# Kernel optimization log

Hardware: AMD Instinct MI355X
Metric: run time of the kernel (lower is better)

Reference implementation:

```python
import jax, jax.numpy as jnp
import numpy as np
from jax import lax

# Dense per-batch layout [B, N, 3]; PyG MLP realized as Linear(+ReLU on all but last layer);
# BatchNorm omitted (eval-mode BN with identity stats is an absorbable affine).
DIMS = {"sa1": [3, 64, 64, 128], "sa2": [131, 128, 128, 256], "sa3": [259, 256, 256, 512], "sa4": [515, 512, 1024]}
B, N, K = 8, 4096, 64  # batch clouds, points per cloud, max neighbors (from radius(..., max_num_neighbors=64))


def setup_inputs() -> dict:
    key = jax.random.key(0)
    inp = {"pos": jax.random.normal(jax.random.fold_in(key, 0), (B, N, 3), jnp.float32)}
    c = 1
    for name, ch in DIMS.items():
        for i in range(len(ch) - 1):
            inp[f"{name}_w{i}"] = jax.random.normal(jax.random.fold_in(key, c), (ch[i], ch[i + 1]), jnp.float32) / np.sqrt(ch[i])
            inp[f"{name}_b{i}"] = jnp.zeros((ch[i + 1],), jnp.float32)
            c += 1
    return inp


def _mlp(x, params):
    n = len(params)
    for i, (W, b) in enumerate(params):
        x = x @ W + b
        if i < n - 1:  # plain last layer (PyG MLP plain_last=True)
            x = jax.nn.relu(x)
    return x


def _fps(pos, n_sample):
    # farthest point sampling, deterministic start at index 0; pos [N,3]
    Np = pos.shape[0]
    def step(carry, _):
        min_d, cur = carry
        d = jnp.sum((pos - pos[cur]) ** 2, axis=-1)
        min_d = jnp.minimum(min_d, d)
        return (min_d, jnp.argmax(min_d).astype(jnp.int32)), cur
    _, idx = lax.scan(step, (jnp.full((Np,), 1e30, pos.dtype), jnp.int32(0)), None, length=n_sample)
    return idx  # [n_sample]


def _sa(x, pos, ratio, r, params):
    # SAModule: fps -> radius ball query (K nearest within r) -> PointNetConv (gather-MLP-scatter-max)
    S = int(pos.shape[1] * ratio)
    idx = jax.vmap(lambda p: _fps(p, S))(pos)                       # [B,S]
    pos_dst = jnp.take_along_axis(pos, idx[:, :, None], axis=1)     # [B,S,3]
    d2 = jnp.sum((pos_dst[:, :, None, :] - pos[:, None, :, :]) ** 2, axis=-1)  # [B,S,N]
    negd, nidx = lax.top_k(-d2, K)                                  # K nearest neighbors
    valid = (-negd) < r * r                                         # within ball radius (>=1: self at d=0)
    pos_j = jax.vmap(lambda p, i: p[i])(pos, nidx)                  # [B,S,K,3]
    rel = pos_j - pos_dst[:, :, None, :]
    if x is None:
        feat = rel
    else:
        x_j = jax.vmap(lambda a, i: a[i])(x, nidx)                  # [B,S,K,F]
        feat = jnp.concatenate([x_j, rel], axis=-1)
    h = _mlp(feat, params)                                          # [B,S,K,C]
    h = jnp.where(valid[..., None], h, -1e30)
    return jnp.max(h, axis=2), pos_dst                              # scatter-max over neighbors


def _backbone(pos, P):
    x1, pos1 = _sa(None, pos, 0.25, 0.2, P["sa1"])
    x2, pos2 = _sa(x1, pos1, 0.25, 0.4, P["sa2"])
    x3, pos3 = _sa(x2, pos2, 0.25, 0.8, P["sa3"])
    h = _mlp(jnp.concatenate([x3, pos3], axis=-1), P["sa4"])        # GlobalSAModule
    return jnp.max(h, axis=1)                                       # global_max_pool -> [B,1024]


def reference(pos, sa1_w0, sa1_b0, sa1_w1, sa1_b1, sa1_w2, sa1_b2, sa2_w0, sa2_b0, sa2_w1, sa2_b1, sa2_w2, sa2_b2, sa3_w0, sa3_b0, sa3_w1, sa3_b1, sa3_w2, sa3_b2, sa4_w0, sa4_b0, sa4_w1, sa4_b1):
    P = {
        "sa1": [(sa1_w0, sa1_b0), (sa1_w1, sa1_b1), (sa1_w2, sa1_b2)],
        "sa2": [(sa2_w0, sa2_b0), (sa2_w1, sa2_b1), (sa2_w2, sa2_b2)],
        "sa3": [(sa3_w0, sa3_b0), (sa3_w1, sa3_b1), (sa3_w2, sa3_b2)],
        "sa4": [(sa4_w0, sa4_b0), (sa4_w1, sa4_b1)],
    }
    return _backbone(pos, P)
```

## Files before the change

### kernel.cpp

```cpp
#include <hip/hip_runtime.h>

#define DEV __device__ __forceinline__

DEV float d2_exact(float ax, float ay, float az, float bx, float by, float bz) {
    float dx = __fadd_rn(ax, -bx);
    float dy = __fadd_rn(ay, -by);
    float dz = __fadd_rn(az, -bz);
    return __fadd_rn(__fadd_rn(__fmul_rn(dx, dx), __fmul_rn(dy, dy)), __fmul_rn(dz, dz));
}

DEV unsigned long long umax64(unsigned long long a, unsigned long long b) { return a > b ? a : b; }
DEV unsigned long long umin64(unsigned long long a, unsigned long long b) { return a < b ? a : b; }

template <int CTRL>
DEV float dpp_fmax(float x) {
    const int xi = __float_as_int(x);
    const int yi = __builtin_amdgcn_update_dpp(xi, xi, CTRL, 0xF, 0xF, false);
    return fmaxf(x, __int_as_float(yi));
}

DEV float wave_fmax_bcast(float x) {
    x = dpp_fmax<0x111>(x);
    x = dpp_fmax<0x112>(x);
    x = dpp_fmax<0x114>(x);
    x = dpp_fmax<0x118>(x);
    x = dpp_fmax<0x142>(x);
    x = dpp_fmax<0x143>(x);
    return __int_as_float(__builtin_amdgcn_readlane(__float_as_int(x), 63));
}

template <int N, int S, int T>
__global__ __launch_bounds__(T) void fps_kernel(const float* __restrict__ pos,
                                                float* __restrict__ pos_out) {
    constexpr int C  = N / T;
    constexpr int NW = T / 64;
    __shared__ float sx[N], sy[N], sz[N];
    __shared__ unsigned long long sred[2][NW];
    const int b = blockIdx.x, t = threadIdx.x;
    const float* p = pos + (size_t)b * N * 3;
    for (int i = t; i < N; i += T) { sx[i] = p[3*i]; sy[i] = p[3*i+1]; sz[i] = p[3*i+2]; }
    __syncthreads();
    float px[C], py[C], pz[C], md[C];
    const int base = t * C;
#pragma unroll
    for (int i = 0; i < C; i++) { px[i]=sx[base+i]; py[i]=sy[base+i]; pz[i]=sz[base+i]; md[i]=1e30f; }
    float cx = sx[0], cy = sy[0], cz = sz[0];
    const int lane = t & 63, wave = t >> 6;
    for (int s = 0; s < S; s++) {
        if (t == 0) {
            float* po = pos_out + ((size_t)b * S + s) * 3;
            po[0] = cx; po[1] = cy; po[2] = cz;
        }
        float bv = -1.0f; int bi = 0;
#pragma unroll
        for (int i = 0; i < C; i++) {
            float d = d2_exact(px[i], py[i], pz[i], cx, cy, cz);
            float m = fminf(md[i], d);
            md[i] = m;
            if (m > bv) { bv = m; bi = base + i; }
        }
        const float wm = wave_fmax_bcast(bv);
        const unsigned long long eq = __ballot(bv == wm);
        const int srcl = __ffsll(eq) - 1;
        const int wbi  = __builtin_amdgcn_readlane(bi, srcl);
        if (lane == 0)
            sred[s & 1][wave] = ((unsigned long long)__float_as_uint(wm) << 32) |
                                (unsigned long long)(unsigned int)(~wbi);
        __syncthreads();
        unsigned long long v = sred[s & 1][0];
#pragma unroll
        for (int w = 1; w < NW; w++) v = umax64(v, sred[s & 1][w]);
        const int cur = (int)(~(unsigned int)v);
        cx = sx[cur]; cy = sy[cur]; cz = sz[cur];
    }
}

template <int NSRC, int T>
__global__ __launch_bounds__(T) void ballq_kernel(const float* __restrict__ pos_src,
                                                  const float* __restrict__ pos_dst,
                                                  const int S, const float rsq,
                                                  int* __restrict__ nidx, int* __restrict__ ncnt) {
    __shared__ float d2s[NSRC];
    __shared__ int scnt, sfill;
    __shared__ unsigned long long sred[T / 64];
    const int bs = blockIdx.x, t = threadIdx.x;
    const int b = bs / S;
    const float* pd = pos_dst + (size_t)bs * 3;
    const float qx = pd[0], qy = pd[1], qz = pd[2];
    const float* ps = pos_src + (size_t)b * NSRC * 3;
    if (t == 0) { scnt = 0; sfill = 0; }
    __syncthreads();
    int lc = 0;
    for (int j = t; j < NSRC; j += T) {
        float d2 = d2_exact(ps[3*j], ps[3*j+1], ps[3*j+2], qx, qy, qz);
        d2s[j] = d2;
        lc += (d2 < rsq) ? 1 : 0;
    }
    if (lc) atomicAdd(&scnt, lc);
    __syncthreads();
    const int c = scnt;
    int* mi = nidx + (size_t)bs * 64;
    if (c <= 64) {
        if (t == 0) ncnt[bs] = c;
        for (int j = t; j < NSRC; j += T) {
            if (d2s[j] < rsq) { int p = atomicAdd(&sfill, 1); mi[p] = j; }
        }
    } else {
        if (t == 0) ncnt[bs] = 64;
        const int lane = t & 63, wave = t >> 6;
        for (int k = 0; k < 64; k++) {
            unsigned long long best = ~0ULL;
            for (int j = t; j < NSRC; j += T) {
                unsigned long long key =
                    ((unsigned long long)__float_as_uint(d2s[j]) << 32) | (unsigned int)j;
                best = umin64(best, key);
            }
#pragma unroll
            for (int o = 32; o >= 1; o >>= 1) best = umin64(best, __shfl_xor(best, o, 64));
            if (lane == 0) sred[wave] = best;
            __syncthreads();
            if (t == 0) {
                unsigned long long v = sred[0];
                for (int w = 1; w < T / 64; w++) v = umin64(v, sred[w]);
                int j = (int)(unsigned int)v;
                mi[k] = j;
                d2s[j] = __uint_as_float(0x7F800000u);
            }
            __syncthreads();
        }
    }
}

#define LP 68

template <int RPT>
DEV void fma_step(const float* __restrict__ inT, const float (*wt)[64],
                  const int cig, const int ci, const int tr, const int tc,
                  float (&acc)[RPT][4]) {
    const float4 w = *(const float4*)(&wt[ci][4 * tc]);
    const float wv[4] = {w.x, w.y, w.z, w.w};
    if constexpr (RPT == 4) {
        const float4 a = *(const float4*)(inT + (size_t)cig * LP + 4 * tr);
        const float av[4] = {a.x, a.y, a.z, a.w};
#pragma unroll
        for (int i = 0; i < 4; i++)
#pragma unroll
            for (int j = 0; j < 4; j++) acc[i][j] = fmaf(av[i], wv[j], acc[i][j]);
    } else {
        const float2 a = *(const float2*)(inT + (size_t)cig * LP + 2 * tr);
        const float av[2] = {a.x, a.y};
#pragma unroll
        for (int i = 0; i < 2; i++)
#pragma unroll
            for (int j = 0; j < 4; j++) acc[i][j] = fmaf(av[i], wv[j], acc[i][j]);
    }
}

template <int CIN, int COUT, bool RELU, int TT>
DEV void gemm_tile(const float* __restrict__ inT, const float* __restrict__ W,
                   const float* __restrict__ bias, float* __restrict__ outT,
                   float (*wt)[64], const int t) {
    constexpr int RPT  = 1024 / TT;
    constexpr int NCH  = CIN / 32;
    constexpr int TAIL = CIN % 32;
    const int tc = t & 15, tr = t >> 4;
    for (int co0 = 0; co0 < COUT; co0 += 64) {
        float acc[RPT][4] = {};
        for (int ch = 0; ch < NCH; ch++) {
            const int ci0 = ch * 32;
            __syncthreads();
            for (int e = t; e < 2048; e += TT) {
                const int co = e & 63, ci = e >> 6;
                wt[ci][co] = W[(size_t)(ci0 + ci) * COUT + co0 + co];
            }
            __syncthreads();
#pragma unroll 4
            for (int ci = 0; ci < 32; ci++)
                fma_step<RPT>(inT, (const float(*)[64])wt, ci0 + ci, ci, tr, tc, acc);
        }
        if constexpr (TAIL > 0) {
            constexpr int ci0 = NCH * 32;
            __syncthreads();
            for (int e = t; e < TAIL * 64; e += TT) {
                const int co = e & 63, ci = e >> 6;
                wt[ci][co] = W[(size_t)(ci0 + ci) * COUT + co0 + co];
            }
            __syncthreads();
#pragma unroll
            for (int ci = 0; ci < TAIL; ci++)
                fma_step<RPT>(inT, (const float(*)[64])wt, ci0 + ci, ci, tr, tc, acc);
        }
#pragma unroll
        for (int j = 0; j < 4; j++) {
            const float bj = bias[co0 + 4 * tc + j];
            if constexpr (RPT == 4) {
                float4 o;
                o.x = acc[0][j] + bj; o.y = acc[1][j] + bj;
                o.z = acc[2][j] + bj; o.w = acc[3][j] + bj;
                if (RELU) {
                    o.x = fmaxf(o.x, 0.f); o.y = fmaxf(o.y, 0.f);
                    o.z = fmaxf(o.z, 0.f); o.w = fmaxf(o.w, 0.f);
                }
                *(float4*)(outT + (size_t)(co0 + 4 * tc + j) * LP + 4 * tr) = o;
            } else {
                float2 o;
                o.x = acc[0][j] + bj; o.y = acc[1][j] + bj;
                if (RELU) { o.x = fmaxf(o.x, 0.f); o.y = fmaxf(o.y, 0.f); }
                *(float2*)(outT + (size_t)(co0 + 4 * tc + j) * LP + 2 * tr) = o;
            }
        }
    }
}

template <int CIN, int COUT, int TT>
DEV void gemm_maxout(const float* __restrict__ inT, const float* __restrict__ W,
                     const float* __restrict__ bias, float* __restrict__ outg,
                     float (*wt)[64], float (*colred)[64], const int t, const int c) {
    constexpr int RPT = 1024 / TT;
    constexpr int NW  = TT / 64;
    constexpr int NCH = CIN / 32;
    const int tc = t & 15, tr = t >> 4, wave = t >> 6;
    for (int co0 = 0; co0 < COUT; co0 += 64) {
        float acc[RPT][4] = {};
        for (int ch = 0; ch < NCH; ch++) {
            const int ci0 = ch * 32;
            __syncthreads();
            for (int e = t; e < 2048; e += TT) {
                const int co = e & 63, ci = e >> 6;
                wt[ci][co] = W[(size_t)(ci0 + ci) * COUT + co0 + co];
            }
            __syncthreads();
#pragma unroll 4
            for (int ci = 0; ci < 32; ci++)
                fma_step<RPT>(inT, (const float(*)[64])wt, ci0 + ci, ci, tr, tc, acc);
        }
        float vr[4];
#pragma unroll
        for (int j = 0; j < 4; j++) {
            const float bj = bias[co0 + 4 * tc + j];
            float m = -1e30f;
#pragma unroll
            for (int i = 0; i < RPT; i++) {
                const float v = acc[i][j] + bj;
                if (RPT * tr + i < c) m = fmaxf(m, v);
            }
            m = fmaxf(m, __shfl_xor(m, 16, 64));
            m = fmaxf(m, __shfl_xor(m, 32, 64));
            vr[j] = m;
        }
        if ((t & 48) == 0) {
#pragma unroll
            for (int j = 0; j < 4; j++) colred[wave][4 * tc + j] = vr[j];
        }
        __syncthreads();
        if (t < 64) {
            float m = colred[0][t];
#pragma unroll
            for (int w = 1; w < NW; w++) m = fmaxf(m, colred[w][t]);
            outg[co0 + t] = m;
        }
        __syncthreads();
    }
}

template <int CX, int C0, int C1, int C2, int NSRC, int TT>
__global__ __launch_bounds__(TT) void sa_conv_kernel(
    const float* __restrict__ x_src, const float* __restrict__ pos_src,
    const float* __restrict__ pos_dst, const int* __restrict__ nidx,
    const int* __restrict__ ncnt,
    const float* __restrict__ w0, const float* __restrict__ b0,
    const float* __restrict__ w1, const float* __restrict__ b1,
    const float* __restrict__ w2, const float* __restrict__ b2,
    float* __restrict__ x_out, const int S) {
    constexpr int CIN = CX + 3;
    constexpr int AR  = (CIN > C1) ? CIN : C1;
    __shared__ float bufA[AR * LP];
    __shared__ float bufB[C0 * LP];
    __shared__ float wt[32][64];
    __shared__ float colred[TT / 64][64];
    const int bs = blockIdx.x, t = threadIdx.x;
    const int b = bs / S;
    const int c = ncnt[bs];
    const int* ni = nidx + (size_t)bs * 64;
    const float* pd = pos_dst + (size_t)bs * 3;
    const float qx = pd[0], qy = pd[1], qz = pd[2];
    if constexpr (CX > 0) {
        constexpr int LG = (CX == 256) ? 8 : 7;
#pragma unroll 4
        for (int e = t; e < 64 * CX; e += TT) {
            const int ci = e & (CX - 1), k = e >> LG;
            float v = 0.f;
            if (k < c) v = x_src[((size_t)b * NSRC + ni[k]) * CX + ci];
            bufA[(size_t)ci * LP + k] = v;
        }
    }
    for (int e = t; e < 192; e += TT) {
        const int k = e & 63, ci = e >> 6;
        float v = 0.f;
        if (k < c) {
            const float* pj = pos_src + ((size_t)b * NSRC + ni[k]) * 3;
            v = (ci == 0 ? pj[0] - qx : (ci == 1 ? pj[1] - qy : pj[2] - qz));
        }
        bufA[(size_t)(CX + ci) * LP + k] = v;
    }
    __syncthreads();
    gemm_tile<CIN, C0, true, TT>(bufA, w0, b0, bufB, wt, t);
    __syncthreads();
    gemm_tile<C0, C1, true, TT>(bufB, w1, b1, bufA, wt, t);
    __syncthreads();
    gemm_maxout<C1, C2, TT>(bufA, w2, b2, x_out + (size_t)bs * C2, wt, colred, t, c);
}

__global__ __launch_bounds__(256) void gsa1_kernel(const float* __restrict__ x3,
                                                   const float* __restrict__ pos3,
                                                   const float* __restrict__ w0,
                                                   const float* __restrict__ b0,
                                                   float* __restrict__ h1) {
    __shared__ float at[32][LP];
    __shared__ float wt[32][64];
    const int b = blockIdx.x >> 3, co0 = (blockIdx.x & 7) * 64;
    const int t = threadIdx.x, tc = t & 15, tr = t >> 4;
    float acc[4][4] = {};
    for (int ci0 = 0; ci0 < 515; ci0 += 32) {
        const int cc = (515 - ci0) < 32 ? (515 - ci0) : 32;
        __syncthreads();
        for (int e = t; e < cc * 64; e += 256) {
            const int k = e & 63, ci = e >> 6, cig = ci0 + ci;
            at[ci][k] = (cig < 512) ? x3[((size_t)b * 64 + k) * 512 + cig]
                                    : pos3[((size_t)b * 64 + k) * 3 + (cig - 512)];
        }
        for (int e = t; e < cc * 64; e += 256) {
            const int co = e & 63, ci = e >> 6;
            wt[ci][co] = w0[(size_t)(ci0 + ci) * 512 + co0 + co];
        }
        __syncthreads();
#pragma unroll 4
        for (int ci = 0; ci < 32; ci++) {
            if (ci >= cc) break;
            const float4 a = *(const float4*)&at[ci][4 * tr];
            const float4 w = *(const float4*)&wt[ci][4 * tc];
            const float av[4] = {a.x, a.y, a.z, a.w};
            const float wv[4] = {w.x, w.y, w.z, w.w};
#pragma unroll
            for (int i = 0; i < 4; i++)
#pragma unroll
                for (int j = 0; j < 4; j++) acc[i][j] = fmaf(av[i], wv[j], acc[i][j]);
        }
    }
#pragma unroll
    for (int j = 0; j < 4; j++) {
        const float bj = b0[co0 + 4 * tc + j];
#pragma unroll
        for (int i = 0; i < 4; i++) {
            float v = acc[i][j] + bj;
            v = fmaxf(v, 0.f);
            h1[((size_t)b * 64 + 4 * tr + i) * 512 + co0 + 4 * tc + j] = v;
        }
    }
}

__global__ __launch_bounds__(256) void gsa2_kernel(const float* __restrict__ h1,
                                                   const float* __restrict__ w1,
                                                   const float* __restrict__ b1,
                                                   float* __restrict__ out) {
    __shared__ float at[32][LP];
    __shared__ float wt[32][64];
    __shared__ float colred[4][64];
    const int b = blockIdx.x >> 4, co0 = (blockIdx.x & 15) * 64;
    const int t = threadIdx.x, tc = t & 15, tr = t >> 4, wave = t >> 6;
    float acc[4][4] = {};
    for (int ci0 = 0; ci0 < 512; ci0 += 32) {
        __syncthreads();
        for (int e = t; e < 32 * 64; e += 256) {
            const int k = e & 63, ci = e >> 6;
            at[ci][k] = h1[((size_t)b * 64 + k) * 512 + ci0 + ci];
        }
        for (int e = t; e < 32 * 64; e += 256) {
            const int co = e & 63, ci = e >> 6;
            wt[ci][co] = w1[(size_t)(ci0 + ci) * 1024 + co0 + co];
        }
        __syncthreads();
#pragma unroll 4
        for (int ci = 0; ci < 32; ci++) {
            const float4 a = *(const float4*)&at[ci][4 * tr];
            const float4 w = *(const float4*)&wt[ci][4 * tc];
            const float av[4] = {a.x, a.y, a.z, a.w};
            const float wv[4] = {w.x, w.y, w.z, w.w};
#pragma unroll
            for (int i = 0; i < 4; i++)
#pragma unroll
                for (int j = 0; j < 4; j++) acc[i][j] = fmaf(av[i], wv[j], acc[i][j]);
        }
    }
    float vr[4];
#pragma unroll
    for (int j = 0; j < 4; j++) {
        const float bj = b1[co0 + 4 * tc + j];
        float m = -1e30f;
#pragma unroll
        for (int i = 0; i < 4; i++) m = fmaxf(m, acc[i][j] + bj);
        m = fmaxf(m, __shfl_xor(m, 16, 64));
        m = fmaxf(m, __shfl_xor(m, 32, 64));
        vr[j] = m;
    }
    if ((t & 48) == 0) {
#pragma unroll
        for (int j = 0; j < 4; j++) colred[wave][4 * tc + j] = vr[j];
    }
    __syncthreads();
    if (t < 64) {
        const float m = fmaxf(fmaxf(colred[0][t], colred[1][t]),
                              fmaxf(colred[2][t], colred[3][t]));
        out[(size_t)b * 1024 + co0 + t] = m;
    }
}

extern "C" void kernel_launch(void* const* d_in, const int* in_sizes, int n_in,
                              void* d_out, int out_size, void* d_ws, size_t ws_size,
                              hipStream_t stream) {
    (void)in_sizes; (void)n_in; (void)out_size; (void)ws_size;
    const float* pos    = (const float*)d_in[0];
    const float* sa1_w0 = (const float*)d_in[1];  const float* sa1_b0 = (const float*)d_in[2];
    const float* sa1_w1 = (const float*)d_in[3];  const float* sa1_b1 = (const float*)d_in[4];
    const float* sa1_w2 = (const float*)d_in[5];  const float* sa1_b2 = (const float*)d_in[6];
    const float* sa2_w0 = (const float*)d_in[7];  const float* sa2_b0 = (const float*)d_in[8];
    const float* sa2_w1 = (const float*)d_in[9];  const float* sa2_b1 = (const float*)d_in[10];
    const float* sa2_w2 = (const float*)d_in[11]; const float* sa2_b2 = (const float*)d_in[12];
    const float* sa3_w0 = (const float*)d_in[13]; const float* sa3_b0 = (const float*)d_in[14];
    const float* sa3_w1 = (const float*)d_in[15]; const float* sa3_b1 = (const float*)d_in[16];
    const float* sa3_w2 = (const float*)d_in[17]; const float* sa3_b2 = (const float*)d_in[18];
    const float* sa4_w0 = (const float*)d_in[19]; const float* sa4_b0 = (const float*)d_in[20];
    const float* sa4_w1 = (const float*)d_in[21]; const float* sa4_b1 = (const float*)d_in[22];
    float* out = (float*)d_out;
    char* ws = (char*)d_ws;

    float* pos1 = (float*)(ws + 0);
    float* pos2 = (float*)(ws + 98304);
    float* pos3 = (float*)(ws + 122880);
    float* x1   = (float*)(ws + 129024);
    float* x2   = (float*)(ws + 4323328);
    float* x3   = (float*)(ws + 6420480);
    int* nidx1  = (int*)(ws + 7469056);
    int* ncnt1  = (int*)(ws + 9566208);
    int* nidx2  = (int*)(ws + 9598976);
    int* ncnt2  = (int*)(ws + 10123264);
    int* nidx3  = (int*)(ws + 10131456);
    int* ncnt3  = (int*)(ws + 10262528);
    float* h1g  = (float*)(ws + 10264576);

    const float rsq1 = (float)(0.2 * 0.2);
    const float rsq2 = (float)(0.4 * 0.4);
    const float rsq3 = (float)(0.8 * 0.8);

    fps_kernel<4096, 1024, 256><<<dim3(8), dim3(256), 0, stream>>>(pos, pos1);
    fps_kernel<1024, 256, 256><<<dim3(8), dim3(256), 0, stream>>>(pos1, pos2);
    fps_kernel<256, 64, 256><<<dim3(8), dim3(256), 0, stream>>>(pos2, pos3);

    ballq_kernel<4096, 256><<<dim3(8 * 1024), dim3(256), 0, stream>>>(pos, pos1, 1024, rsq1, nidx1, ncnt1);
    ballq_kernel<1024, 256><<<dim3(8 * 256), dim3(256), 0, stream>>>(pos1, pos2, 256, rsq2, nidx2, ncnt2);
    ballq_kernel<256, 256><<<dim3(8 * 64), dim3(256), 0, stream>>>(pos2, pos3, 64, rsq3, nidx3, ncnt3);

    sa_conv_kernel<0, 64, 64, 128, 4096, 256><<<dim3(8 * 1024), dim3(256), 0, stream>>>(
        nullptr, pos, pos1, nidx1, ncnt1, sa1_w0, sa1_b0, sa1_w1, sa1_b1, sa1_w2, sa1_b2, x1, 1024);
    sa_conv_kernel<128, 128, 128, 256, 1024, 256><<<dim3(8 * 256), dim3(256), 0, stream>>>(
        x1, pos1, pos2, nidx2, ncnt2, sa2_w0, sa2_b0, sa2_w1, sa2_b1, sa2_w2, sa2_b2, x2, 256);
    sa_conv_kernel<256, 256, 256, 512, 256, 512><<<dim3(8 * 64), dim3(512), 0, stream>>>(
        x2, pos2, pos3, nidx3, ncnt3, sa3_w0, sa3_b0, sa3_w1, sa3_b1, sa3_w2, sa3_b2, x3, 64);

    gsa1_kernel<<<dim3(64), dim3(256), 0, stream>>>(x3, pos3, sa4_w0, sa4_b0, h1g);
    gsa2_kernel<<<dim3(128), dim3(256), 0, stream>>>(h1g, sa4_w1, sa4_b1, out);
}
```

Measured before the change: 1.916 ms.

## Restructure per-centroid MLP to lane-per-neighbor with scalar-broadcast weight loads

Replaces the shared-memory-tiled 4x4 register GEMM with a scheme where each lane owns one neighbor row and each wave computes 16 output channels. Weights are read directly from global memory at wave-uniform addresses (the wave index goes through readfirstlane, so these can become scalar loads), which removes the LDS weight staging and its block barriers. The final layer max-reduces over neighbors with DPP wave reductions instead of a cross-wave LDS reduction. This trades LDS data reuse for many more global/scalar weight loads per FMA, and leaves fewer independent accumulator rows per thread.

Result: faster. 1.798 ms (-6.2%).

```diff
diff --git a/kernel.cpp b/kernel.cpp
--- a/kernel.cpp
+++ b/kernel.cpp
@@ -131,135 +131,83 @@
     }
 }
 
-#define LP 68
-
-template <int RPT>
-DEV void fma_step(const float* __restrict__ inT, const float (*wt)[64],
-                  const int cig, const int ci, const int tr, const int tc,
-                  float (&acc)[RPT][4]) {
-    const float4 w = *(const float4*)(&wt[ci][4 * tc]);
-    const float wv[4] = {w.x, w.y, w.z, w.w};
-    if constexpr (RPT == 4) {
-        const float4 a = *(const float4*)(inT + (size_t)cig * LP + 4 * tr);
-        const float av[4] = {a.x, a.y, a.z, a.w};
-#pragma unroll
-        for (int i = 0; i < 4; i++)
-#pragma unroll
-            for (int j = 0; j < 4; j++) acc[i][j] = fmaf(av[i], wv[j], acc[i][j]);
-    } else {
-        const float2 a = *(const float2*)(inT + (size_t)cig * LP + 2 * tr);
-        const float av[2] = {a.x, a.y};
-#pragma unroll
-        for (int i = 0; i < 2; i++)
-#pragma unroll
-            for (int j = 0; j < 4; j++) acc[i][j] = fmaf(av[i], wv[j], acc[i][j]);
-    }
-}
+#define AST 65
 
 template <int CIN, int COUT, bool RELU, int TT>
-DEV void gemm_tile(const float* __restrict__ inT, const float* __restrict__ W,
-                   const float* __restrict__ bias, float* __restrict__ outT,
-                   float (*wt)[64], const int t) {
-    constexpr int RPT  = 1024 / TT;
-    constexpr int NCH  = CIN / 32;
-    constexpr int TAIL = CIN % 32;
-    const int tc = t & 15, tr = t >> 4;
-    for (int co0 = 0; co0 < COUT; co0 += 64) {
-        float acc[RPT][4] = {};
-        for (int ch = 0; ch < NCH; ch++) {
-            const int ci0 = ch * 32;
-            __syncthreads();
-            for (int e = t; e < 2048; e += TT) {
-                const int co = e & 63, ci = e >> 6;
-                wt[ci][co] = W[(size_t)(ci0 + ci) * COUT + co0 + co];
-            }
-            __syncthreads();
-#pragma unroll 4
-            for (int ci = 0; ci < 32; ci++)
-                fma_step<RPT>(inT, (const float(*)[64])wt, ci0 + ci, ci, tr, tc, acc);
-        }
-        if constexpr (TAIL > 0) {
-            constexpr int ci0 = NCH * 32;
-            __syncthreads();
-            for (int e = t; e < TAIL * 64; e += TT) {
-                const int co = e & 63, ci = e >> 6;
-                wt[ci][co] = W[(size_t)(ci0 + ci) * COUT + co0 + co];
-            }
-            __syncthreads();
-#pragma unroll
-            for (int ci = 0; ci < TAIL; ci++)
-                fma_step<RPT>(inT, (const float(*)[64])wt, ci0 + ci, ci, tr, tc, acc);
-        }
-#pragma unroll
-        for (int j = 0; j < 4; j++) {
-            const float bj = bias[co0 + 4 * tc + j];
-            if constexpr (RPT == 4) {
-                float4 o;
-                o.x = acc[0][j] + bj; o.y = acc[1][j] + bj;
-                o.z = acc[2][j] + bj; o.w = acc[3][j] + bj;
-                if (RELU) {
-                    o.x = fmaxf(o.x, 0.f); o.y = fmaxf(o.y, 0.f);
-                    o.z = fmaxf(o.z, 0.f); o.w = fmaxf(o.w, 0.f);
-                }
-                *(float4*)(outT + (size_t)(co0 + 4 * tc + j) * LP + 4 * tr) = o;
-            } else {
-                float2 o;
-                o.x = acc[0][j] + bj; o.y = acc[1][j] + bj;
-                if (RELU) { o.x = fmaxf(o.x, 0.f); o.y = fmaxf(o.y, 0.f); }
-                *(float2*)(outT + (size_t)(co0 + 4 * tc + j) * LP + 2 * tr) = o;
-            }
+DEV void layer_fc(const float* __restrict__ inA, const float* __restrict__ W,
+                  const float* __restrict__ bias, float* __restrict__ outA,
+                  const int wav, const int lane) {
+    constexpr int PASS = (TT / 64) * 16;
+    for (int cb0 = 0; cb0 < COUT; cb0 += PASS) {
+        const int cb = cb0 + wav * 16;
+        const float* __restrict__ wp = W + cb;
+        float acc[16] = {};
+        int ci = 0;
+        for (; ci + 4 <= CIN; ci += 4) {
+            const float a0 = inA[(ci + 0) * AST + lane];
+            const float a1 = inA[(ci + 1) * AST + lane];
+            const float a2 = inA[(ci + 2) * AST + lane];
+            const float a3 = inA[(ci + 3) * AST + lane];
+#pragma unroll
+            for (int j = 0; j < 16; j++) acc[j] = fmaf(a0, wp[(size_t)(ci + 0) * COUT + j], acc[j]);
+#pragma unroll
+            for (int j = 0; j < 16; j++) acc[j] = fmaf(a1, wp[(size_t)(ci + 1) * COUT + j], acc[j]);
+#pragma unroll
+            for (int j = 0; j < 16; j++) acc[j] = fmaf(a2, wp[(size_t)(ci + 2) * COUT + j], acc[j]);
+#pragma unroll
+            for (int j = 0; j < 16; j++) acc[j] = fmaf(a3, wp[(size_t)(ci + 3) * COUT + j], acc[j]);
+        }
+        for (; ci < CIN; ci++) {
+            const float a0 = inA[ci * AST + lane];
+#pragma unroll
+            for (int j = 0; j < 16; j++) acc[j] = fmaf(a0, wp[(size_t)ci * COUT + j], acc[j]);
+        }
+#pragma unroll
+        for (int j = 0; j < 16; j++) {
+            float v = acc[j] + bias[cb + j];
+            if (RELU) v = fmaxf(v, 0.f);
+            outA[(size_t)(cb + j) * AST + lane] = v;
         }
     }
 }
 
 template <int CIN, int COUT, int TT>
-DEV void gemm_maxout(const float* __restrict__ inT, const float* __restrict__ W,
-                     const float* __restrict__ bias, float* __restrict__ outg,
-                     float (*wt)[64], float (*colred)[64], const int t, const int c) {
-    constexpr int RPT = 1024 / TT;
-    constexpr int NW  = TT / 64;
-    constexpr int NCH = CIN / 32;
-    const int tc = t & 15, tr = t >> 4, wave = t >> 6;
-    for (int co0 = 0; co0 < COUT; co0 += 64) {
-        float acc[RPT][4] = {};
-        for (int ch = 0; ch < NCH; ch++) {
-            const int ci0 = ch * 32;
-            __syncthreads();
-            for (int e = t; e < 2048; e += TT) {
-                const int co = e & 63, ci = e >> 6;
-                wt[ci][co] = W[(size_t)(ci0 + ci) * COUT + co0 + co];
-            }
-            __syncthreads();
-#pragma unroll 4
-            for (int ci = 0; ci < 32; ci++)
-                fma_step<RPT>(inT, (const float(*)[64])wt, ci0 + ci, ci, tr, tc, acc);
-        }
-        float vr[4];
-#pragma unroll
-        for (int j = 0; j < 4; j++) {
-            const float bj = bias[co0 + 4 * tc + j];
-            float m = -1e30f;
-#pragma unroll
-            for (int i = 0; i < RPT; i++) {
-                const float v = acc[i][j] + bj;
-                if (RPT * tr + i < c) m = fmaxf(m, v);
-            }
-            m = fmaxf(m, __shfl_xor(m, 16, 64));
-            m = fmaxf(m, __shfl_xor(m, 32, 64));
-            vr[j] = m;
-        }
-        if ((t & 48) == 0) {
-#pragma unroll
-            for (int j = 0; j < 4; j++) colred[wave][4 * tc + j] = vr[j];
-        }
-        __syncthreads();
-        if (t < 64) {
-            float m = colred[0][t];
-#pragma unroll
-            for (int w = 1; w < NW; w++) m = fmaxf(m, colred[w][t]);
-            outg[co0 + t] = m;
-        }
-        __syncthreads();
+DEV void layer_max(const float* __restrict__ inA, const float* __restrict__ W,
+                   const float* __restrict__ bias, float* __restrict__ outg,
+                   const int wav, const int lane, const int c) {
+    constexpr int PASS = (TT / 64) * 16;
+    for (int cb0 = 0; cb0 < COUT; cb0 += PASS) {
+        const int cb = cb0 + wav * 16;
+        const float* __restrict__ wp = W + cb;
+        float acc[16] = {};
+        int ci = 0;
+        for (; ci + 4 <= CIN; ci += 4) {
+            const float a0 = inA[(ci + 0) * AST + lane];
+            const float a1 = inA[(ci + 1) * AST + lane];
+            const float a2 = inA[(ci + 2) * AST + lane];
+            const float a3 = inA[(ci + 3) * AST + lane];
+#pragma unroll
+            for (int j = 0; j < 16; j++) acc[j] = fmaf(a0, wp[(size_t)(ci + 0) * COUT + j], acc[j]);
+#pragma unroll
+            for (int j = 0; j < 16; j++) acc[j] = fmaf(a1, wp[(size_t)(ci + 1) * COUT + j], acc[j]);
+#pragma unroll
+            for (int j = 0; j < 16; j++) acc[j] = fmaf(a2, wp[(size_t)(ci + 2) * COUT + j], acc[j]);
+#pragma unroll
+            for (int j = 0; j < 16; j++) acc[j] = fmaf(a3, wp[(size_t)(ci + 3) * COUT + j], acc[j]);
+        }
+        for (; ci < CIN; ci++) {
+            const float a0 = inA[ci * AST + lane];
+#pragma unroll
+            for (int j = 0; j < 16; j++) acc[j] = fmaf(a0, wp[(size_t)ci * COUT + j], acc[j]);
+        }
+        float vout = 0.f;
+#pragma unroll
+        for (int j = 0; j < 16; j++) {
+            const float v = (lane < c) ? acc[j] + bias[cb + j] : -1e30f;
+            const float m = wave_fmax_bcast(v);
+            if (lane == j) vout = m;
+        }
+        if (lane < 16) outg[cb + lane] = vout;
     }
 }
 
@@ -274,42 +222,45 @@
     float* __restrict__ x_out, const int S) {
     constexpr int CIN = CX + 3;
     constexpr int AR  = (CIN > C1) ? CIN : C1;
-    __shared__ float bufA[AR * LP];
-    __shared__ float bufB[C0 * LP];
-    __shared__ float wt[32][64];
-    __shared__ float colred[TT / 64][64];
+    __shared__ float bufA[AR * AST];
+    __shared__ float bufB[C0 * AST];
+    __shared__ int sni[64];
     const int bs = blockIdx.x, t = threadIdx.x;
     const int b = bs / S;
     const int c = ncnt[bs];
-    const int* ni = nidx + (size_t)bs * 64;
     const float* pd = pos_dst + (size_t)bs * 3;
     const float qx = pd[0], qy = pd[1], qz = pd[2];
+    if (t < 64) sni[t] = nidx[(size_t)bs * 64 + t];
+    __syncthreads();
     if constexpr (CX > 0) {
         constexpr int LG = (CX == 256) ? 8 : 7;
-#pragma unroll 4
         for (int e = t; e < 64 * CX; e += TT) {
             const int ci = e & (CX - 1), k = e >> LG;
             float v = 0.f;
-            if (k < c) v = x_src[((size_t)b * NSRC + ni[k]) * CX + ci];
-            bufA[(size_t)ci * LP + k] = v;
+            if (k < c) v = x_src[((size_t)b * NSRC + sni[k]) * CX + ci];
+            bufA[ci * AST + k] = v;
         }
     }
     for (int e = t; e < 192; e += TT) {
         const int k = e & 63, ci = e >> 6;
         float v = 0.f;
         if (k < c) {
-            const float* pj = pos_src + ((size_t)b * NSRC + ni[k]) * 3;
+            const float* pj = pos_src + ((size_t)b * NSRC + sni[k]) * 3;
             v = (ci == 0 ? pj[0] - qx : (ci == 1 ? pj[1] - qy : pj[2] - qz));
         }
-        bufA[(size_t)(CX + ci) * LP + k] = v;
-    }
-    __syncthreads();
-    gemm_tile<CIN, C0, true, TT>(bufA, w0, b0, bufB, wt, t);
-    __syncthreads();
-    gemm_tile<C0, C1, true, TT>(bufB, w1, b1, bufA, wt, t);
-    __syncthreads();
-    gemm_maxout<C1, C2, TT>(bufA, w2, b2, x_out + (size_t)bs * C2, wt, colred, t, c);
-}
+        bufA[(CX + ci) * AST + k] = v;
+    }
+    __syncthreads();
+    const int wav  = __builtin_amdgcn_readfirstlane(t >> 6);
+    const int lane = t & 63;
+    layer_fc<CIN, C0, true, TT>(bufA, w0, b0, bufB, wav, lane);
+    __syncthreads();
+    layer_fc<C0, C1, true, TT>(bufB, w1, b1, bufA, wav, lane);
+    __syncthreads();
+    layer_max<C1, C2, TT>(bufA, w2, b2, x_out + (size_t)bs * C2, wav, lane, c);
+}
+
+#define LP 68
 
 __global__ __launch_bounds__(256) void gsa1_kernel(const float* __restrict__ x3,
                                                    const float* __restrict__ pos3,
```
